# Kernel tuning notes

Hardware: AMD Instinct MI355X
Metric: run time of the kernel (lower is better)

Reference implementation:

```python
import jax, jax.numpy as jnp
import numpy as np

OBS_DIM, ACT_DIM, HID_DIM, FEAT = 256, 32, 1024, 512
T_STEPS, BATCH = 64, 512
LOG2PI = float(np.log(2.0 * np.pi))


def _mlp(h, w0, b0, w1, b1, w2, b2):
    # 2 hidden elu layers + linear head (MLPDecoder mean; fix_std Normal, std=1)
    x = jax.nn.elu(h @ w0.T + b0)
    x = jax.nn.elu(x @ w1.T + b1)
    return x @ w2.T + b2


def _gru(x, h, w_ih, w_hh, b_ih, b_hh):
    # torch.nn.GRUCell semantics
    gi = x @ w_ih.T + b_ih
    gh = h @ w_hh.T + b_hh
    i_r, i_z, i_n = jnp.split(gi, 3, axis=-1)
    h_r, h_z, h_n = jnp.split(gh, 3, axis=-1)
    r = jax.nn.sigmoid(i_r + h_r)
    z = jax.nn.sigmoid(i_z + h_z)
    n = jnp.tanh(i_n + r * h_n)
    return (1.0 - z) * n + z * h


def setup_inputs() -> dict:
    key = jax.random.key(0)
    ks = jax.random.split(key, 20)
    d = {}
    d['obs'] = jax.random.normal(ks[0], (T_STEPS, BATCH, OBS_DIM), jnp.float32)
    d['action'] = jax.random.normal(ks[1], (T_STEPS, BATCH, ACT_DIM), jnp.float32)
    d['reward'] = jax.random.normal(ks[2], (T_STEPS, BATCH, 1), jnp.float32)
    in_dim = OBS_DIM + ACT_DIM
    s = lambda fan_in: 1.0 / np.sqrt(fan_in)
    d['gru_w_ih'] = jax.random.normal(ks[3], (3 * HID_DIM, in_dim), jnp.float32) * s(in_dim)
    d['gru_w_hh'] = jax.random.normal(ks[4], (3 * HID_DIM, HID_DIM), jnp.float32) * s(HID_DIM)
    d['gru_b_ih'] = jnp.zeros((3 * HID_DIM,), jnp.float32)
    d['gru_b_hh'] = jnp.zeros((3 * HID_DIM,), jnp.float32)
    for name, out_dim, base in (('obs', OBS_DIM, 5), ('rew', 1, 11)):
        d[f'{name}_w0'] = jax.random.normal(ks[base], (FEAT, HID_DIM), jnp.float32) * s(HID_DIM)
        d[f'{name}_b0'] = jnp.zeros((FEAT,), jnp.float32)
        d[f'{name}_w1'] = jax.random.normal(ks[base + 1], (FEAT, FEAT), jnp.float32) * s(FEAT)
        d[f'{name}_b1'] = jnp.zeros((FEAT,), jnp.float32)
        d[f'{name}_w2'] = jax.random.normal(ks[base + 2], (out_dim, FEAT), jnp.float32) * s(FEAT)
        d[f'{name}_b2'] = jnp.zeros((out_dim,), jnp.float32)
    return d


def reference(obs, action, reward,
              gru_w_ih, gru_w_hh, gru_b_ih, gru_b_hh,
              obs_w0, obs_b0, obs_w1, obs_b1, obs_w2, obs_b2,
              rew_w0, rew_b0, rew_w1, rew_b1, rew_w2, rew_b2):
    T, B = obs.shape[0], obs.shape[1]

    def normal_logprob_sum(x, mean):
        # Normal(mean, std=1): -0.5*(x-mean)^2 - 0.5*log(2*pi), summed
        return -0.5 * jnp.sum((x - mean) ** 2 + LOG2PI)

    h0 = _gru(jnp.concatenate([obs[0], jnp.zeros_like(action[0])], axis=1),
              jnp.zeros((B, HID_DIM), obs.dtype),
              gru_w_ih, gru_w_hh, gru_b_ih, gru_b_hh)

    def step(h, xs):
        obs_t, act_t, rew_t = xs
        obs_mean = _mlp(h, obs_w0, obs_b0, obs_w1, obs_b1, obs_w2, obs_b2)
        lp_obs = normal_logprob_sum(obs_t, obs_mean)
        rew_mean = _mlp(h, rew_w0, rew_b0, rew_w1, rew_b1, rew_w2, rew_b2)
        lp_rew = normal_logprob_sum(rew_t, rew_mean)
        # feed predicted obs (mode) + ground-truth action back into the GRU
        x = jnp.concatenate([obs_mean, act_t], axis=1)
        h_next = _gru(x, h, gru_w_ih, gru_w_hh, gru_b_ih, gru_b_hh)
        return h_next, (obs_mean, rew_mean, lp_obs, lp_rew)

    _, (pre_obs, pre_reward, lp_obs, lp_rew) = jax.lax.scan(
        step, h0, (obs, action, reward))

    denom = jnp.asarray(T * B, obs.dtype)
    pre_obs_loss = -jnp.sum(lp_obs) / denom
    pre_reward_loss = -jnp.sum(lp_rew) / denom
    loss = pre_obs_loss + pre_reward_loss  # action_mimic=False -> action loss is 0
    return loss, pre_obs, pre_reward
```

## Files before the change

kernel.cpp:

```cpp
#include <hip/hip_runtime.h>
#include <stdint.h>

#define T_STEPS 64
#define BATCH   512
#define OBS_DIM 256
#define ACT_DIM 32
#define HID     1024
#define FEAT    512
#define GDIM    3072
#define KIH     288
#define NBLK    256
#define GMEMB   32
#define LOG2PI  1.8378770664093453f
#define HWREG_XCC_ID 14356

typedef __attribute__((ext_vector_type(8))) short  short8;
typedef __attribute__((ext_vector_type(4))) float  floatx4;
typedef __attribute__((ext_vector_type(4))) unsigned int uintx4;
typedef unsigned long long ull;

__device__ __forceinline__ float bf2f(unsigned int u) {
    return __uint_as_float(u << 16);
}
__device__ __forceinline__ unsigned int f2bf(float f) {
    unsigned int u = __float_as_uint(f);
    return (u + 0x7FFFu + ((u >> 16) & 1u)) >> 16;
}
// ... 60 lines not shown
        int prev = __hip_atomic_fetch_add(cnt, 1, __ATOMIC_RELAXED,
                                          __HIP_MEMORY_SCOPE_AGENT);
        if (prev == members * epoch - 1) {
            __hip_atomic_store(gen, epoch, __ATOMIC_RELAXED,
                               __HIP_MEMORY_SCOPE_AGENT);
        } else {
            while (__hip_atomic_load(gen, __ATOMIC_RELAXED,
                                     __HIP_MEMORY_SCOPE_AGENT) < epoch)
                __builtin_amdgcn_s_sleep(2);
        }
        __builtin_amdgcn_fence(__ATOMIC_ACQUIRE, "workgroup");
    }
    __syncthreads();
}

template<bool COH>
__device__ __forceinline__ void s1_stage(const P& p, unsigned short* lds,
                                         int g, int m,
                                         const unsigned short* hbf_r,
                                         unsigned short* Z1_w,
                                         unsigned short* GHb_w) {
    const int tid = threadIdx.x, lane = tid & 63, wv = tid >> 6;
    const int wr = wv & 1, wc = wv >> 1, fr = lane & 15, fq = lane >> 4;
    const int rowg = g * 64, col0 = m * 128;
    unsigned short* ldsA = lds;
    unsigned short* ldsB = lds + 64 * 136;

    floatx4 acc[2][4];
    floatx4 z4 = {0.f, 0.f, 0.f, 0.f};
#pragma unroll
    for (int mi = 0; mi < 2; ++mi)
#pragma unroll
        for (int n = 0; n < 4; ++n) acc[mi][n] = z4;

    const ull* Aq = (const ull*)(hbf_r + (size_t)rowg * HID);
    const unsigned short* Bg = p.Ws1 + (size_t)col0 * HID;

    ull apf[8];
#pragma unroll
    for (int j = 0; j < 8; ++j) { int f = tid + 256 * j;
        apf[j] = a_ld64<COH>(Aq + (size_t)(f >> 5) * 256 + (f & 31)); }
    uintx4 rb0[4], rb1[4];
#pragma unroll
    for (int i = 0; i < 4; ++i) { int c = tid + 256 * i;
        const unsigned short* bp = Bg + (size_t)(c >> 3) * HID + ((c & 7) << 3);
        rb0[i] = __builtin_nontemporal_load((const uintx4*)bp);
        rb1[i] = __builtin_nontemporal_load((const uintx4*)(bp + 64)); }

#define S1_MFMA(ASUB)                                                          \
    {                                                                          \
        _Pragma("unroll")                                                      \
        for (int ks = 0; ks < 2; ++ks) {                                       \
            short8 af[2], bf8[4];                                              \
            _Pragma("unroll")                                                  \
            for (int mi = 0; mi < 2; ++mi)                                     \
                af[mi] = *(const short8*)(ldsA + (wr * 32 + mi * 16 + fr) * 136 + (ASUB) + ks * 32 + fq * 8); \
            _Pragma("unroll")                                                  \
            for (int n = 0; n < 4; ++n)                                        \
                bf8[n] = *(const short8*)(ldsB + (wc * 64 + n * 16 + fr) * 72 + ks * 32 + fq * 8); \
            _Pragma("unroll")                                                  \
            for (int mi = 0; mi < 2; ++mi)                                     \
                _Pragma("unroll")                                              \
                for (int n = 0; n < 4; ++n)                                    \
                    acc[mi][n] = __builtin_amdgcn_mfma_f32_16x16x32_bf16(      \
                        af[mi], bf8[n], acc[mi][n], 0, 0, 0);                  \
        }                                                                      \
    }

    for (int it2 = 0; it2 < 8; ++it2) {
        bar_fast();
#pragma unroll
        for (int j = 0; j < 8; ++j) { int f = tid + 256 * j;
            *(ull*)(ldsA + (size_t)(f >> 5) * 136 + ((f & 31) << 2)) = apf[j]; }
#pragma unroll
        for (int i = 0; i < 4; ++i) { int c = tid + 256 * i;
            *(uintx4*)(ldsB + (c >> 3) * 72 + ((c & 7) << 3)) = rb0[i]; }
        bar_lds();
        if (it2 < 7) {
            int c2 = it2 + 1;
#pragma unroll
            for (int j = 0; j < 8; ++j) { int f = tid + 256 * j;
                apf[j] = a_ld64<COH>(Aq + (size_t)(f >> 5) * 256 + c2 * 32 + (f & 31)); }
            int k0n = (2 * it2 + 2) * 64;
#pragma unroll
            for (int i = 0; i < 4; ++i) { int c = tid + 256 * i;
                rb0[i] = __builtin_nontemporal_load((const uintx4*)
                    (Bg + (size_t)(c >> 3) * HID + k0n + ((c & 7) << 3))); }
        }
        S1_MFMA(0);
        bar_fast();
#pragma unroll
        for (int i = 0; i < 4; ++i) { int c = tid + 256 * i;
            *(uintx4*)(ldsB + (c >> 3) * 72 + ((c & 7) << 3)) = rb1[i]; }
        bar_lds();
        if (it2 < 7) {
            int k0n = (2 * it2 + 3) * 64;
#pragma unroll
            for (int i = 0; i < 4; ++i) { int c = tid + 256 * i;
                rb1[i] = __builtin_nontemporal_load((const uintx4*)
                    (Bg + (size_t)(c >> 3) * HID + k0n + ((c & 7) << 3))); }
        }
        S1_MFMA(64);
    }
#undef S1_MFMA

    const bool isZ1 = (col0 < 1024);
#pragma unroll
    for (int mi = 0; mi < 2; ++mi)
#pragma unroll
        for (int n = 0; n < 4; ++n)
#pragma unroll
            for (int j = 0; j < 4; ++j) {
                int row = rowg + wr * 32 + mi * 16 + fq * 4 + j;
                int col = col0 + wc * 64 + n * 16 + fr;
                float v = acc[mi][n][j] + p.bias_s1[col];
                unsigned int ow = f2bf(isZ1 ? elu1(v) : v);
                unsigned int pr = __shfl_xor(ow, 1, 64);
                if (!(fr & 1)) {
                    unsigned int pk = ow | (pr << 16);
                    if (isZ1)
                        a_st<COH>((unsigned int*)(Z1_w + row * HID + col), pk);
                    else
                        a_st<COH>((unsigned int*)GHb_w + (size_t)row * 1536 + ((col - 1024) >> 1), pk);
                }
            }
}

template<bool COH>
__device__ __forceinline__ void s2_stage(const P& p, unsigned short* lds,
                                         int g, int m,
                                         const unsigned short* Z1_r,
                                         unsigned short* Z2_w) {
    const int tid = threadIdx.x, lane = tid & 63, wv = tid >> 6;
    const int wr = wv & 1, wc = wv >> 1, fr = lane & 15, fq = lane >> 4;
    const int rowg = g * 64;
    const int z = m >> 4, col0 = (m & 15) * 32;
    unsigned short* ldsA = lds;
    unsigned short* ldsB = lds + 64 * 136;

    floatx4 acc[2];
    floatx4 z4 = {0.f, 0.f, 0.f, 0.f};
    acc[0] = z4; acc[1] = z4;

    const ull* Aq = (const ull*)(Z1_r + (size_t)rowg * HID + z * FEAT);
    const unsigned short* Bg = (z ? p.W1r : p.W1o) + (size_t)col0 * FEAT;
    const float* bias = z ? p.b1r : p.b1o;

    ull apf[8];
#pragma unroll
    for (int j = 0; j < 8; ++j) { int f = tid + 256 * j;
        apf[j] = a_ld64<COH>(Aq + (size_t)(f >> 5) * 256 + (f & 31)); }
    const unsigned short* bp0 = Bg + (size_t)(tid >> 3) * FEAT + ((tid & 7) << 3);
    uintx4 rb0 = *(const uintx4*)(bp0);
    uintx4 rb1 = *(const uintx4*)(bp0 + 64);

#define S2_MFMA(ASUB)                                                          \
    {                                                                          \
        _Pragma("unroll")                                                      \
        for (int ks = 0; ks < 2; ++ks) {                                       \
            short8 bf8 = *(const short8*)(ldsB + (wc * 16 + fr) * 72 + ks * 32 + fq * 8); \
            _Pragma("unroll")                                                  \
            for (int mi = 0; mi < 2; ++mi) {                                   \
                short8 af = *(const short8*)(ldsA + (wr * 32 + mi * 16 + fr) * 136 + (ASUB) + ks * 32 + fq * 8); \
                acc[mi] = __builtin_amdgcn_mfma_f32_16x16x32_bf16(af, bf8, acc[mi], 0, 0, 0); \
            }                                                                  \
        }                                                                      \
    }

    for (int it2 = 0; it2 < 4; ++it2) {
        bar_fast();
#pragma unroll
        for (int j = 0; j < 8; ++j) { int f = tid + 256 * j;
            *(ull*)(ldsA + (size_t)(f >> 5) * 136 + ((f & 31) << 2)) = apf[j]; }
        *(uintx4*)(ldsB + (tid >> 3) * 72 + ((tid & 7) << 3)) = rb0;
        bar_lds();
        if (it2 < 3) {
            int c2 = it2 + 1;
#pragma unroll
            for (int j = 0; j < 8; ++j) { int f = tid + 256 * j;
                apf[j] = a_ld64<COH>(Aq + (size_t)(f >> 5) * 256 + c2 * 32 + (f & 31)); }
            rb0 = *(const uintx4*)(bp0 + (2 * it2 + 2) * 64);
        }
        S2_MFMA(0);
        bar_fast();
        *(uintx4*)(ldsB + (tid >> 3) * 72 + ((tid & 7) << 3)) = rb1;
        bar_lds();
        if (it2 < 3) rb1 = *(const uintx4*)(bp0 + (2 * it2 + 3) * 64);
        S2_MFMA(64);
    }
#undef S2_MFMA

#pragma unroll
    for (int mi = 0; mi < 2; ++mi)
#pragma unroll
        for (int j = 0; j < 4; ++j) {
            int row = rowg + wr * 32 + mi * 16 + fq * 4 + j;
            int col = col0 + wc * 16 + fr;
            float v = acc[mi][j] + bias[col];
            unsigned int ow = f2bf(elu1(v));
            unsigned int pr = __shfl_xor(ow, 1, 64);
            if (!(fr & 1))
                a_st<COH>((unsigned int*)(Z2_w + row * HID + z * FEAT + col), ow | (pr << 16));
        }
}

template<bool COH>
__device__ __forceinline__ void s3_stage(const P& p, unsigned short* lds,
                                         int g, int m, int t,
                                         const unsigned short* Z2_r,
                                         unsigned short* Xbuf_w) {
    const int tid = threadIdx.x, lane = tid & 63, wv = tid >> 6;
    const int wr = wv & 1, wc = wv >> 1, fr = lane & 15, fq = lane >> 4;
    const int rowg = g * 64;

    if (m < 8) {
        const int col0 = m * 32;
        unsigned short* ldsA = lds;
        unsigned short* ldsB = lds + 64 * 136;
        floatx4 acc[2];
        floatx4 z4 = {0.f, 0.f, 0.f, 0.f};
        acc[0] = z4; acc[1] = z4;

        const ull* Aq = (const ull*)(Z2_r + (size_t)rowg * HID);
        const unsigned short* Bg = p.W2o + (size_t)col0 * FEAT;

        ull apf[8];
#pragma unroll
        for (int j = 0; j < 8; ++j) { int f = tid + 256 * j;
            apf[j] = a_ld64<COH>(Aq + (size_t)(f >> 5) * 256 + (f & 31)); }
        const unsigned short* bp0 = Bg + (size_t)(tid >> 3) * FEAT + ((tid & 7) << 3);
        uintx4 rb0 = *(const uintx4*)(bp0);
        uintx4 rb1 = *(const uintx4*)(bp0 + 64);

#define S3_MFMA(ASUB)                                                          \
        {                                                                      \
            _Pragma("unroll")                                                  \
            for (int ks = 0; ks < 2; ++ks) {                                   \
                short8 bf8 = *(const short8*)(ldsB + (wc * 16 + fr) * 72 + ks * 32 + fq * 8); \
                _Pragma("unroll")                                              \
                for (int mi = 0; mi < 2; ++mi) {                               \
                    short8 af = *(const short8*)(ldsA + (wr * 32 + mi * 16 + fr) * 136 + (ASUB) + ks * 32 + fq * 8); \
                    acc[mi] = __builtin_amdgcn_mfma_f32_16x16x32_bf16(af, bf8, acc[mi], 0, 0, 0); \
                }                                                              \
            }                                                                  \
        }

        for (int it2 = 0; it2 < 4; ++it2) {
            bar_fast();
#pragma unroll
            for (int j = 0; j < 8; ++j) { int f = tid + 256 * j;
                *(ull*)(ldsA + (size_t)(f >> 5) * 136 + ((f & 31) << 2)) = apf[j]; }
            *(uintx4*)(ldsB + (tid >> 3) * 72 + ((tid & 7) << 3)) = rb0;
            bar_lds();
            if (it2 < 3) {
                int c2 = it2 + 1;
#pragma unroll
                for (int j = 0; j < 8; ++j) { int f = tid + 256 * j;
                    apf[j] = a_ld64<COH>(Aq + (size_t)(f >> 5) * 256 + c2 * 32 + (f & 31)); }
                rb0 = *(const uintx4*)(bp0 + (2 * it2 + 2) * 64);
            }
            S3_MFMA(0);
            bar_fast();
            *(uintx4*)(ldsB + (tid >> 3) * 72 + ((tid & 7) << 3)) = rb1;
            bar_lds();
            if (it2 < 3) rb1 = *(const uintx4*)(bp0 + (2 * it2 + 3) * 64);
            S3_MFMA(64);
        }
#undef S3_MFMA

        const int col = col0 + wc * 16 + fr;
        const float b2oc = p.b2o[col];
        float lsum = 0.f;
#pragma unroll
        for (int mi = 0; mi < 2; ++mi)
#pragma unroll
            for (int j = 0; j < 4; ++j) {
                int row = rowg + wr * 32 + mi * 16 + fq * 4 + j;
                float mval = acc[mi][j] + b2oc;
                size_t oidx = (size_t)t * BATCH * OBS_DIM + (size_t)row * OBS_DIM + col;
                __builtin_nontemporal_store(mval, p.out + 1 + oidx);
                unsigned int ow = f2bf(mval);
                unsigned int pr = __shfl_xor(ow, 1, 64);
                if (!(fr & 1))
                    a_st<COH>((unsigned int*)(Xbuf_w + row * KIH + col), ow | (pr << 16));
                float d = __builtin_nontemporal_load(p.obs + oidx) - mval;
                lsum += d * d;
            }
#pragma unroll
        for (int off = 32; off > 0; off >>= 1) lsum += __shfl_down(lsum, off, 64);
        if (lane == 0) atomicAdd(p.accum + 0, lsum);
    } else if (m == 8) {
        for (int e = tid; e < 64 * 16; e += 256) {
            int row = rowg + (e >> 4), cp = (e & 15) * 2;
            const float* ap = p.action + ((size_t)t * BATCH + row) * ACT_DIM + cp;
            unsigned int lo = f2bf(__builtin_nontemporal_load(ap));
            unsigned int hi = f2bf(__builtin_nontemporal_load(ap + 1));
            a_st<COH>((unsigned int*)(Xbuf_w + row * KIH + OBS_DIM + cp), lo | (hi << 16));
        }
    } else if (m >= 16) {
        const int row = rowg + (m - 16) * 4 + wv;
        const ull* zq = (const ull*)(Z2_r + (size_t)row * HID + FEAT) + lane * 2;
        ull z0 = a_ld64<COH>(zq);
        ull z1 = a_ld64<COH>(zq + 1);
        short8 w8 = *(const short8*)(p.w2r + lane * 8);
        float s = 0.f;
#pragma unroll
        for (int k = 0; k < 4; ++k) {
            unsigned int u = (unsigned int)(z0 >> (16 * k)) & 0xFFFFu;
            s += bf2f(u) * bf2f((unsigned int)(unsigned short)w8[k]);
        }
#pragma unroll
        for (int k = 0; k < 4; ++k) {
            unsigned int u = (unsigned int)(z1 >> (16 * k)) & 0xFFFFu;
            s += bf2f(u) * bf2f((unsigned int)(unsigned short)w8[4 + k]);
// ... 6 lines not shown
                mm, p.out + 1 + (size_t)T_STEPS * BATCH * OBS_DIM + (size_t)t * BATCH + row);
            float d = __builtin_nontemporal_load(p.reward + (size_t)t * BATCH + row) - mm;
            atomicAdd(p.accum + 1, d * d);
        }
    }
}

template<bool COH>
__device__ __forceinline__ void s4_stage(const P& p, unsigned short* lds,
                                         int g, int m, int use_gh,
                                         const unsigned short* Xbuf_r,
                                         const unsigned short* GHb_r,
                                         const float* h_r,
                                         float* h_w, unsigned short* hbf_w) {
    const int tid = threadIdx.x, lane = tid & 63, wv = tid >> 6;
    const int wr = wv & 1, wc = wv >> 1, fr = lane & 15, fq = lane >> 4;
    const int rowg = g * 64;
    const int col0 = m * 32;
    unsigned short* ldsA = lds;
    unsigned short* ldsB = lds + 64 * 104;

    floatx4 acc[3][2];
    floatx4 z4 = {0.f, 0.f, 0.f, 0.f};
#pragma unroll
    for (int g3 = 0; g3 < 3; ++g3) { acc[g3][0] = z4; acc[g3][1] = z4; }

    const ull* Xq = (const ull*)(Xbuf_r + (size_t)rowg * KIH);
    ull apf[6];
#pragma unroll
    for (int j = 0; j < 6; ++j) { int f = tid + 256 * j;
        apf[j] = a_ld64<COH>(Xq + (size_t)(f / 24) * 72 + (f % 24)); }

    uintx4 wpfA[5], wpfB[5];
#pragma unroll
    for (int j = 0; j < 5; ++j) { int f = tid + 256 * j;
        if (f < 1152) { int r = f / 12, ko = (f - r * 12) * 8;
            const unsigned short* wp =
                p.Wih + (size_t)((r >> 5) * HID + col0 + (r & 31)) * KIH + ko;
            wpfA[j] = __builtin_nontemporal_load((const uintx4*)wp);
            wpfB[j] = __builtin_nontemporal_load((const uintx4*)(wp + 96)); } }

#pragma unroll
    for (int c = 0; c < 3; ++c) {
        bar_fast();
#pragma unroll
        for (int j = 0; j < 6; ++j) { int f = tid + 256 * j;
            *(ull*)(ldsA + (size_t)(f / 24) * 104 + ((f % 24) << 2)) = apf[j]; }
#pragma unroll
        for (int j = 0; j < 5; ++j) { int f = tid + 256 * j;
            if (f < 1152) { int r = f / 12, ko = (f - r * 12) * 8;
                *(uintx4*)(ldsB + r * 104 + ko) = (c & 1) ? wpfB[j] : wpfA[j]; } }
        bar_lds();
        if (c < 2) {
#pragma unroll
            for (int j = 0; j < 6; ++j) { int f = tid + 256 * j;
                apf[j] = a_ld64<COH>(Xq + (size_t)(f / 24) * 72 + (c + 1) * 24 + (f % 24)); }
        }
        if (c == 0) {
#pragma unroll
            for (int j = 0; j < 5; ++j) { int f = tid + 256 * j;
                if (f < 1152) { int r = f / 12, ko = (f - r * 12) * 8;
                    wpfA[j] = __builtin_nontemporal_load((const uintx4*)
                        (p.Wih + (size_t)((r >> 5) * HID + col0 + (r & 31)) * KIH + 192 + ko)); } }
        }
#pragma unroll
        for (int ks = 0; ks < 3; ++ks) {
            short8 af[2];
#pragma unroll
            for (int mi = 0; mi < 2; ++mi)
                af[mi] = *(const short8*)(ldsA + (wr * 32 + mi * 16 + fr) * 104 + ks * 32 + fq * 8);
#pragma unroll
            for (int g3 = 0; g3 < 3; ++g3) {
                short8 bf8 = *(const short8*)(ldsB + (g3 * 32 + wc * 16 + fr) * 104 + ks * 32 + fq * 8);
#pragma unroll
                for (int mi = 0; mi < 2; ++mi)
                    acc[g3][mi] = __builtin_amdgcn_mfma_f32_16x16x32_bf16(
                        af[mi], bf8, acc[g3][mi], 0, 0, 0);
            }
        }
    }

    const int col = col0 + wc * 16 + fr;
    const float bir = p.b_ih[col];
    const float biz = p.b_ih[HID + col];
    const float bin = p.b_ih[2 * HID + col];
    float hrv[2][4], hzv[2][4], hnv[2][4], hpv[2][4];
    if (use_gh) {
        const unsigned int* GW = (const unsigned int*)GHb_r;
        const int cw = col >> 1, hi = col & 1;
#pragma unroll
        for (int mi = 0; mi < 2; ++mi)
#pragma unroll
            for (int j = 0; j < 4; ++j) {
                int row = rowg + wr * 32 + mi * 16 + fq * 4 + j;
                unsigned int ur = a_ld<COH>(GW + (size_t)row * 1536 + cw);
                unsigned int uz = a_ld<COH>(GW + (size_t)row * 1536 + 512 + cw);
                unsigned int un = a_ld<COH>(GW + (size_t)row * 1536 + 1024 + cw);
                hrv[mi][j] = bf2f(hi ? (ur >> 16) : (ur & 0xFFFFu));
                hzv[mi][j] = bf2f(hi ? (uz >> 16) : (uz & 0xFFFFu));
                hnv[mi][j] = bf2f(hi ? (un >> 16) : (un & 0xFFFFu));
                hpv[mi][j] = __uint_as_float(a_ld<COH>((const unsigned int*)(h_r + (size_t)row * HID + col)));
            }
    } else {
        float br = p.b_hh[col], bz = p.b_hh[HID + col], bn = p.b_hh[2 * HID + col];
#pragma unroll
        for (int mi = 0; mi < 2; ++mi)
#pragma unroll
            for (int j = 0; j < 4; ++j) {
                hrv[mi][j] = br; hzv[mi][j] = bz; hnv[mi][j] = bn; hpv[mi][j] = 0.f;
            }
    }
#pragma unroll
    for (int mi = 0; mi < 2; ++mi)
#pragma unroll
        for (int j = 0; j < 4; ++j) {
            int row = rowg + wr * 32 + mi * 16 + fq * 4 + j;
            float r  = sigm(acc[0][mi][j] + bir + hrv[mi][j]);
            float z  = sigm(acc[1][mi][j] + biz + hzv[mi][j]);
            float nn = tanhf(acc[2][mi][j] + bin + r * hnv[mi][j]);
            float hv = (1.f - z) * nn + z * hpv[mi][j];
            a_st<COH>((unsigned int*)(h_w + (size_t)row * HID + col), __float_as_uint(hv));
            unsigned int ow = f2bf(hv);
            unsigned int pr = __shfl_xor(ow, 1, 64);
            if (!(fr & 1))
                a_st<COH>((unsigned int*)(hbf_w + row * HID + col), ow | (pr << 16));
        }
}

template<bool COH>
__device__ void rollout(const P& p, unsigned short* lds, int g, int m) {
    int* gcnt = p.bar + g * 128;
    int* ggen = p.bar + g * 128 + 64;
    int epoch = 0;

    s4_stage<COH>(p, lds, g, m, 0, p.Xbuf[1], p.GHb[0], p.h[0], p.h[0], p.hbf[0]);
    gbar(gcnt, ggen, epoch, GMEMB);

    for (int t = 0; t < T_STEPS; ++t) {
        const int pr = t & 1, nx = (t + 1) & 1;
        s1_stage<COH>(p, lds, g, m, p.hbf[pr], p.Z1[pr], p.GHb[pr]);
        gbar(gcnt, ggen, epoch, GMEMB);
        s2_stage<COH>(p, lds, g, m, p.Z1[pr], p.Z2[pr]);
        gbar(gcnt, ggen, epoch, GMEMB);
        s3_stage<COH>(p, lds, g, m, t, p.Z2[pr], p.Xbuf[pr]);
        gbar(gcnt, ggen, epoch, GMEMB);
        if (t < T_STEPS - 1) {
            s4_stage<COH>(p, lds, g, m, 1, p.Xbuf[pr], p.GHb[pr], p.h[pr],
                          p.h[nx], p.hbf[nx]);
            gbar(gcnt, ggen, epoch, GMEMB);
        }
    }
}

__global__ __launch_bounds__(256, 1) void k_persist(P p) {
    __shared__ unsigned short lds[17920];
    __shared__ int sh[3];

    const int bid = blockIdx.x;
    if (threadIdx.x == 0) {
        unsigned int xcd = __builtin_amdgcn_s_getreg(HWREG_XCC_ID) & 7u;
        int r = __hip_atomic_fetch_add(p.bar + 1024 + xcd, 1,
                                       __ATOMIC_RELAXED, __HIP_MEMORY_SCOPE_AGENT);
        sh[0] = (int)xcd; sh[1] = r;
    }
    int repoch = 0;
    gbar(p.bar + 1200, p.bar + 1264, repoch, NBLK);
    if (threadIdx.x == 0) {
        int ok = (sh[1] < 32);
        for (int i = 0; i < 8; ++i)
            ok &= (dev_ld((const unsigned int*)(p.bar + 1024 + i)) == 32u);
        sh[2] = ok;
    }
    __syncthreads();

    if (sh[2]) rollout<false>(p, lds, sh[0], sh[1]);
    else       rollout<true >(p, lds, bid & 7, bid >> 3);

    gbar(p.bar + 1200, p.bar + 1264, repoch, NBLK);
    if (bid == 0 && threadIdx.x == 0) {
        const float inv = 1.f / (float)(T_STEPS * BATCH);
        float a0 = dev_ldf(p.accum + 0);
        float a1 = dev_ldf(p.accum + 1);
        p.out[0] = 0.5f * a0 * inv + 128.f * LOG2PI
                 + 0.5f * a1 * inv + 0.5f * LOG2PI;
    }
}

__global__ void k_convert(
    const float* __restrict__ ow0, const float* __restrict__ rw0,
    const float* __restrict__ whh, const float* __restrict__ wih,
    const float* __restrict__ ow1, const float* __restrict__ rw1,
    const float* __restrict__ ow2, const float* __restrict__ rw2,
    const float* __restrict__ ob0, const float* __restrict__ rb0,
    const float* __restrict__ bhh,
// ... 21 lines not shown
    for (int i = i0; i < 4096; i += stride)
        bias_s1[i] = (i < 512) ? ob0[i] : (i < 1024) ? rb0[i - 512] : bhh[i - 1024];
}

__global__ void k_init(const float* __restrict__ obs,
                       unsigned short* __restrict__ Xbuf1,
                       float* __restrict__ accum,
                       int* __restrict__ bar)
{
    int i = blockIdx.x * 256 + threadIdx.x;
    if (i < BATCH * KIH) {
        int row = i / KIH, col = i - row * KIH;
        Xbuf1[i] = (col < OBS_DIM) ? (unsigned short)f2bf(obs[row * OBS_DIM + col])
                                   : (unsigned short)0;
    }
    if (i < 2)    accum[i] = 0.f;
    if (i < 1536) bar[i] = 0;
}

extern "C" void kernel_launch(void* const* d_in, const int* in_sizes, int n_in,
                              void* d_out, int out_size, void* d_ws, size_t ws_size,
                              hipStream_t stream)
{
    const float* obs      = (const float*)d_in[0];
    const float* action   = (const float*)d_in[1];
    const float* reward   = (const float*)d_in[2];
    const float* gru_w_ih = (const float*)d_in[3];
    const float* gru_w_hh = (const float*)d_in[4];
    const float* gru_b_ih = (const float*)d_in[5];
    const float* gru_b_hh = (const float*)d_in[6];
    const float* obs_w0   = (const float*)d_in[7];
    const float* obs_b0   = (const float*)d_in[8];
// ... 22 lines not shown
    unsigned short* w2r  = (unsigned short*)alloc((size_t)FEAT * 2);
    float* bias_s1       = (float*)alloc((size_t)4096 * 4);
    unsigned short* Z1a  = (unsigned short*)alloc((size_t)BATCH * HID * 2);
    unsigned short* Z1b  = (unsigned short*)alloc((size_t)BATCH * HID * 2);
    unsigned short* Z2a  = (unsigned short*)alloc((size_t)BATCH * HID * 2);
    unsigned short* Z2b  = (unsigned short*)alloc((size_t)BATCH * HID * 2);
    unsigned short* GHa  = (unsigned short*)alloc((size_t)BATCH * GDIM * 2);
    unsigned short* GHbB = (unsigned short*)alloc((size_t)BATCH * GDIM * 2);
    unsigned short* Xba  = (unsigned short*)alloc((size_t)BATCH * KIH * 2);
    unsigned short* Xbb  = (unsigned short*)alloc((size_t)BATCH * KIH * 2);
    float* ha            = (float*)alloc((size_t)BATCH * HID * 4);
    float* hb            = (float*)alloc((size_t)BATCH * HID * 4);
    unsigned short* hfa  = (unsigned short*)alloc((size_t)BATCH * HID * 2);
    unsigned short* hfb  = (unsigned short*)alloc((size_t)BATCH * HID * 2);
    float* accum         = (float*)alloc(256);
    int*   bar           = (int*)alloc(8192);

    dim3 blk(256);

    k_convert<<<dim3(1024), blk, 0, stream>>>(
        obs_w0, rew_w0, gru_w_hh, gru_w_ih, obs_w1, rew_w1, obs_w2, rew_w2,
        obs_b0, rew_b0, gru_b_hh, Ws1, Wih, W1o, W1r, W2o, w2r, bias_s1);

    k_init<<<dim3((BATCH * KIH + 255) / 256), blk, 0, stream>>>(obs, Xbb, accum, bar);

    P hp;
    hp.obs = obs; hp.action = action; hp.reward = reward;
    hp.b_ih = gru_b_ih; hp.b_hh = gru_b_hh;
    hp.b1o = obs_b1; hp.b1r = rew_b1; hp.b2o = obs_b2; hp.b2r = rew_b2;
    hp.Ws1 = Ws1; hp.Wih = Wih; hp.W1o = W1o; hp.W1r = W1r;
    hp.W2o = W2o; hp.w2r = w2r; hp.bias_s1 = bias_s1;
    hp.Z1[0] = Z1a; hp.Z1[1] = Z1b;
    hp.Z2[0] = Z2a; hp.Z2[1] = Z2b;
    hp.Xbuf[0] = Xba; hp.Xbuf[1] = Xbb;
    hp.hbf[0] = hfa; hp.hbf[1] = hfb;
    hp.GHb[0] = GHa; hp.GHb[1] = GHbB;
    hp.h[0] = ha; hp.h[1] = hb;
    hp.accum = accum; hp.out = (float*)d_out;
    hp.bar = bar;

    k_persist<<<dim3(NBLK), blk, 0, stream>>>(hp);
}
```

Measured before the change: 2.542 ms.

## Double persistent blocks to 512 with 32-row tiles and flag-based group barriers

Measured after the change: 3.772 ms. +48.4%, slower.

```diff
diff --git a/kernel.cpp b/kernel.cpp
--- a/kernel.cpp
+++ b/kernel.cpp
@@ -9,8 +9,7 @@
 #define FEAT    512
 #define GDIM    3072
 #define KIH     288
-#define NBLK    256
-#define GMEMB   32
+#define NBLK    512
 #define LOG2PI  1.8378770664093453f
 #define HWREG_XCC_ID 14356
 
@@ -101,31 +100,60 @@
     __syncthreads();
 }
 
+__device__ __forceinline__ void gbar_flags(int* fbase, int m, int& epoch) {
+    __syncthreads();
+    epoch++;
+    if (threadIdx.x == 0) {
+        __builtin_amdgcn_fence(__ATOMIC_RELEASE, "workgroup");
+        dev_st((unsigned int*)(fbase + m * 16), (unsigned int)epoch);
+    }
+    if (threadIdx.x < 64) {
+        const unsigned int* fp =
+            (const unsigned int*)(fbase + (threadIdx.x & 31) * 16);
+        while ((int)dev_ld(fp) < epoch) __builtin_amdgcn_s_sleep(4);
+        __builtin_amdgcn_fence(__ATOMIC_ACQUIRE, "workgroup");
+    }
+    __syncthreads();
+}
+
+__device__ __forceinline__ void gbar_all(int* fbase, int a, int& epoch) {
+    __syncthreads();
+    epoch++;
+    if (threadIdx.x == 0) {
+        __builtin_amdgcn_fence(__ATOMIC_RELEASE, "workgroup");
+        dev_st((unsigned int*)(fbase + a * 16), (unsigned int)epoch);
+    }
+    {
+        const unsigned int* fp =
+            (const unsigned int*)(fbase + threadIdx.x * 16);
+        while ((int)dev_ld(fp) < epoch) __builtin_amdgcn_s_sleep(4);
+    }
+    __builtin_amdgcn_fence(__ATOMIC_ACQUIRE, "workgroup");
+    __syncthreads();
+}
+
 template<bool COH>
 __device__ __forceinline__ void s1_stage(const P& p, unsigned short* lds,
                                          int g, int m,
                                          const unsigned short* hbf_r,
                                          unsigned short* Z1_w,
                                          unsigned short* GHb_w) {
-    const int tid = threadIdx.x, lane = tid & 63, wv = tid >> 6;
-    const int wr = wv & 1, wc = wv >> 1, fr = lane & 15, fq = lane >> 4;
-    const int rowg = g * 64, col0 = m * 128;
+    const int tid = threadIdx.x, lane = tid & 63, wc = tid >> 6;
+    const int fr = lane & 15, fq = lane >> 4;
+    const int rowg = g * 32, col0 = m * 128;
     unsigned short* ldsA = lds;
-    unsigned short* ldsB = lds + 64 * 136;
-
-    floatx4 acc[2][4];
+    unsigned short* ldsB = lds + 32 * 136;
+
+    floatx4 acc[2][2];
     floatx4 z4 = {0.f, 0.f, 0.f, 0.f};
-#pragma unroll
-    for (int mi = 0; mi < 2; ++mi)
-#pragma unroll
-        for (int n = 0; n < 4; ++n) acc[mi][n] = z4;
+    acc[0][0] = z4; acc[0][1] = z4; acc[1][0] = z4; acc[1][1] = z4;
 
     const ull* Aq = (const ull*)(hbf_r + (size_t)rowg * HID);
     const unsigned short* Bg = p.Ws1 + (size_t)col0 * HID;
 
-    ull apf[8];
-#pragma unroll
-    for (int j = 0; j < 8; ++j) { int f = tid + 256 * j;
+    ull apf[4];
+#pragma unroll
+    for (int j = 0; j < 4; ++j) { int f = tid + 256 * j;
         apf[j] = a_ld64<COH>(Aq + (size_t)(f >> 5) * 256 + (f & 31)); }
     uintx4 rb0[4], rb1[4];
 #pragma unroll
@@ -136,28 +164,30 @@
 
 #define S1_MFMA(ASUB)                                                          \
     {                                                                          \
+        __builtin_amdgcn_s_setprio(1);                                         \
         _Pragma("unroll")                                                      \
         for (int ks = 0; ks < 2; ++ks) {                                       \
-            short8 af[2], bf8[4];                                              \
+            short8 af[2], bf8[2];                                              \
             _Pragma("unroll")                                                  \
             for (int mi = 0; mi < 2; ++mi)                                     \
-                af[mi] = *(const short8*)(ldsA + (wr * 32 + mi * 16 + fr) * 136 + (ASUB) + ks * 32 + fq * 8); \
+                af[mi] = *(const short8*)(ldsA + (mi * 16 + fr) * 136 + (ASUB) + ks * 32 + fq * 8); \
             _Pragma("unroll")                                                  \
-            for (int n = 0; n < 4; ++n)                                        \
-                bf8[n] = *(const short8*)(ldsB + (wc * 64 + n * 16 + fr) * 72 + ks * 32 + fq * 8); \
+            for (int n = 0; n < 2; ++n)                                        \
+                bf8[n] = *(const short8*)(ldsB + (wc * 32 + n * 16 + fr) * 72 + ks * 32 + fq * 8); \
             _Pragma("unroll")                                                  \
             for (int mi = 0; mi < 2; ++mi)                                     \
                 _Pragma("unroll")                                              \
-                for (int n = 0; n < 4; ++n)                                    \
+                for (int n = 0; n < 2; ++n)                                    \
                     acc[mi][n] = __builtin_amdgcn_mfma_f32_16x16x32_bf16(      \
                         af[mi], bf8[n], acc[mi][n], 0, 0, 0);                  \
         }                                                                      \
+        __builtin_amdgcn_s_setprio(0);                                         \
     }
 
     for (int it2 = 0; it2 < 8; ++it2) {
         bar_fast();
 #pragma unroll
-        for (int j = 0; j < 8; ++j) { int f = tid + 256 * j;
+        for (int j = 0; j < 4; ++j) { int f = tid + 256 * j;
             *(ull*)(ldsA + (size_t)(f >> 5) * 136 + ((f & 31) << 2)) = apf[j]; }
 #pragma unroll
         for (int i = 0; i < 4; ++i) { int c = tid + 256 * i;
@@ -166,7 +196,7 @@
         if (it2 < 7) {
             int c2 = it2 + 1;
 #pragma unroll
-            for (int j = 0; j < 8; ++j) { int f = tid + 256 * j;
+            for (int j = 0; j < 4; ++j) { int f = tid + 256 * j;
                 apf[j] = a_ld64<COH>(Aq + (size_t)(f >> 5) * 256 + c2 * 32 + (f & 31)); }
             int k0n = (2 * it2 + 2) * 64;
 #pragma unroll
@@ -195,11 +225,11 @@
 #pragma unroll
     for (int mi = 0; mi < 2; ++mi)
 #pragma unroll
-        for (int n = 0; n < 4; ++n)
+        for (int n = 0; n < 2; ++n)
 #pragma unroll
             for (int j = 0; j < 4; ++j) {
-                int row = rowg + wr * 32 + mi * 16 + fq * 4 + j;
-                int col = col0 + wc * 64 + n * 16 + fr;
+                int row = rowg + mi * 16 + fq * 4 + j;
+                int col = col0 + wc * 32 + n * 16 + fr;
                 float v = acc[mi][n][j] + p.bias_s1[col];
                 unsigned int ow = f2bf(isZ1 ? elu1(v) : v);
                 unsigned int pr = __shfl_xor(ow, 1, 64);
@@ -219,76 +249,67 @@
                                          const unsigned short* Z1_r,
                                          unsigned short* Z2_w) {
     const int tid = threadIdx.x, lane = tid & 63, wv = tid >> 6;
-    const int wr = wv & 1, wc = wv >> 1, fr = lane & 15, fq = lane >> 4;
-    const int rowg = g * 64;
+    const int wr = wv & 1, wc = wv >> 1;
+    const int fr = lane & 15, fq = lane >> 4;
+    const int rowg = g * 32;
     const int z = m >> 4, col0 = (m & 15) * 32;
     unsigned short* ldsA = lds;
-    unsigned short* ldsB = lds + 64 * 136;
-
-    floatx4 acc[2];
-    floatx4 z4 = {0.f, 0.f, 0.f, 0.f};
-    acc[0] = z4; acc[1] = z4;
+    unsigned short* ldsB = lds + 32 * 136;
+
+    floatx4 acc = {0.f, 0.f, 0.f, 0.f};
 
     const ull* Aq = (const ull*)(Z1_r + (size_t)rowg * HID + z * FEAT);
     const unsigned short* Bg = (z ? p.W1r : p.W1o) + (size_t)col0 * FEAT;
     const float* bias = z ? p.b1r : p.b1o;
 
-    ull apf[8];
-#pragma unroll
-    for (int j = 0; j < 8; ++j) { int f = tid + 256 * j;
+    ull apf[4];
+#pragma unroll
+    for (int j = 0; j < 4; ++j) { int f = tid + 256 * j;
         apf[j] = a_ld64<COH>(Aq + (size_t)(f >> 5) * 256 + (f & 31)); }
     const unsigned short* bp0 = Bg + (size_t)(tid >> 3) * FEAT + ((tid & 7) << 3);
     uintx4 rb0 = *(const uintx4*)(bp0);
     uintx4 rb1 = *(const uintx4*)(bp0 + 64);
 
-#define S2_MFMA(ASUB)                                                          \
-    {                                                                          \
-        _Pragma("unroll")                                                      \
-        for (int ks = 0; ks < 2; ++ks) {                                       \
-            short8 bf8 = *(const short8*)(ldsB + (wc * 16 + fr) * 72 + ks * 32 + fq * 8); \
-            _Pragma("unroll")                                                  \
-            for (int mi = 0; mi < 2; ++mi) {                                   \
-                short8 af = *(const short8*)(ldsA + (wr * 32 + mi * 16 + fr) * 136 + (ASUB) + ks * 32 + fq * 8); \
-                acc[mi] = __builtin_amdgcn_mfma_f32_16x16x32_bf16(af, bf8, acc[mi], 0, 0, 0); \
-            }                                                                  \
-        }                                                                      \
-    }
+#define S23_MFMA(ASUB)                                                         \
+    { _Pragma("unroll")                                                        \
+      for (int ks = 0; ks < 2; ++ks) {                                         \
+        short8 bf8 = *(const short8*)(ldsB + (wc * 16 + fr) * 72 + ks * 32 + fq * 8); \
+        short8 af = *(const short8*)(ldsA + (wr * 16 + fr) * 136 + (ASUB) + ks * 32 + fq * 8); \
+        acc = __builtin_amdgcn_mfma_f32_16x16x32_bf16(af, bf8, acc, 0, 0, 0);  \
+      } }
 
     for (int it2 = 0; it2 < 4; ++it2) {
         bar_fast();
 #pragma unroll
-        for (int j = 0; j < 8; ++j) { int f = tid + 256 * j;
+        for (int j = 0; j < 4; ++j) { int f = tid + 256 * j;
             *(ull*)(ldsA + (size_t)(f >> 5) * 136 + ((f & 31) << 2)) = apf[j]; }
         *(uintx4*)(ldsB + (tid >> 3) * 72 + ((tid & 7) << 3)) = rb0;
         bar_lds();
         if (it2 < 3) {
             int c2 = it2 + 1;
 #pragma unroll
-            for (int j = 0; j < 8; ++j) { int f = tid + 256 * j;
+            for (int j = 0; j < 4; ++j) { int f = tid + 256 * j;
                 apf[j] = a_ld64<COH>(Aq + (size_t)(f >> 5) * 256 + c2 * 32 + (f & 31)); }
             rb0 = *(const uintx4*)(bp0 + (2 * it2 + 2) * 64);
         }
-        S2_MFMA(0);
+        S23_MFMA(0);
         bar_fast();
         *(uintx4*)(ldsB + (tid >> 3) * 72 + ((tid & 7) << 3)) = rb1;
         bar_lds();
         if (it2 < 3) rb1 = *(const uintx4*)(bp0 + (2 * it2 + 3) * 64);
-        S2_MFMA(64);
-    }
-#undef S2_MFMA
-
-#pragma unroll
-    for (int mi = 0; mi < 2; ++mi)
-#pragma unroll
-        for (int j = 0; j < 4; ++j) {
-            int row = rowg + wr * 32 + mi * 16 + fq * 4 + j;
-            int col = col0 + wc * 16 + fr;
-            float v = acc[mi][j] + bias[col];
-            unsigned int ow = f2bf(elu1(v));
-            unsigned int pr = __shfl_xor(ow, 1, 64);
-            if (!(fr & 1))
-                a_st<COH>((unsigned int*)(Z2_w + row * HID + z * FEAT + col), ow | (pr << 16));
-        }
+        S23_MFMA(64);
+    }
+
+#pragma unroll
+    for (int j = 0; j < 4; ++j) {
+        int row = rowg + wr * 16 + fq * 4 + j;
+        int col = col0 + wc * 16 + fr;
+        float v = acc[j] + bias[col];
+        unsigned int ow = f2bf(elu1(v));
+        unsigned int pr = __shfl_xor(ow, 1, 64);
+        if (!(fr & 1))
+            a_st<COH>((unsigned int*)(Z2_w + row * HID + z * FEAT + col), ow | (pr << 16));
+    }
 }
 
 template<bool COH>
@@ -297,94 +318,77 @@
                                          const unsigned short* Z2_r,
                                          unsigned short* Xbuf_w) {
     const int tid = threadIdx.x, lane = tid & 63, wv = tid >> 6;
-    const int wr = wv & 1, wc = wv >> 1, fr = lane & 15, fq = lane >> 4;
-    const int rowg = g * 64;
+    const int wr = wv & 1, wc = wv >> 1;
+    const int fr = lane & 15, fq = lane >> 4;
+    const int rowg = g * 32;
 
     if (m < 8) {
         const int col0 = m * 32;
         unsigned short* ldsA = lds;
-        unsigned short* ldsB = lds + 64 * 136;
-        floatx4 acc[2];
-        floatx4 z4 = {0.f, 0.f, 0.f, 0.f};
-        acc[0] = z4; acc[1] = z4;
+        unsigned short* ldsB = lds + 32 * 136;
+        floatx4 acc = {0.f, 0.f, 0.f, 0.f};
 
         const ull* Aq = (const ull*)(Z2_r + (size_t)rowg * HID);
         const unsigned short* Bg = p.W2o + (size_t)col0 * FEAT;
 
-        ull apf[8];
-#pragma unroll
-        for (int j = 0; j < 8; ++j) { int f = tid + 256 * j;
+        ull apf[4];
+#pragma unroll
+        for (int j = 0; j < 4; ++j) { int f = tid + 256 * j;
             apf[j] = a_ld64<COH>(Aq + (size_t)(f >> 5) * 256 + (f & 31)); }
         const unsigned short* bp0 = Bg + (size_t)(tid >> 3) * FEAT + ((tid & 7) << 3);
         uintx4 rb0 = *(const uintx4*)(bp0);
         uintx4 rb1 = *(const uintx4*)(bp0 + 64);
 
-#define S3_MFMA(ASUB)                                                          \
-        {                                                                      \
-            _Pragma("unroll")                                                  \
-            for (int ks = 0; ks < 2; ++ks) {                                   \
-                short8 bf8 = *(const short8*)(ldsB + (wc * 16 + fr) * 72 + ks * 32 + fq * 8); \
-                _Pragma("unroll")                                              \
-                for (int mi = 0; mi < 2; ++mi) {                               \
-                    short8 af = *(const short8*)(ldsA + (wr * 32 + mi * 16 + fr) * 136 + (ASUB) + ks * 32 + fq * 8); \
-                    acc[mi] = __builtin_amdgcn_mfma_f32_16x16x32_bf16(af, bf8, acc[mi], 0, 0, 0); \
-                }                                                              \
-            }                                                                  \
-        }
-
         for (int it2 = 0; it2 < 4; ++it2) {
             bar_fast();
 #pragma unroll
-            for (int j = 0; j < 8; ++j) { int f = tid + 256 * j;
+            for (int j = 0; j < 4; ++j) { int f = tid + 256 * j;
                 *(ull*)(ldsA + (size_t)(f >> 5) * 136 + ((f & 31) << 2)) = apf[j]; }
             *(uintx4*)(ldsB + (tid >> 3) * 72 + ((tid & 7) << 3)) = rb0;
             bar_lds();
             if (it2 < 3) {
                 int c2 = it2 + 1;
 #pragma unroll
-                for (int j = 0; j < 8; ++j) { int f = tid + 256 * j;
+                for (int j = 0; j < 4; ++j) { int f = tid + 256 * j;
                     apf[j] = a_ld64<COH>(Aq + (size_t)(f >> 5) * 256 + c2 * 32 + (f & 31)); }
                 rb0 = *(const uintx4*)(bp0 + (2 * it2 + 2) * 64);
             }
-            S3_MFMA(0);
+            S23_MFMA(0);
             bar_fast();
             *(uintx4*)(ldsB + (tid >> 3) * 72 + ((tid & 7) << 3)) = rb1;
             bar_lds();
             if (it2 < 3) rb1 = *(const uintx4*)(bp0 + (2 * it2 + 3) * 64);
-            S3_MFMA(64);
-        }
-#undef S3_MFMA
+            S23_MFMA(64);
+        }
 
         const int col = col0 + wc * 16 + fr;
         const float b2oc = p.b2o[col];
         float lsum = 0.f;
 #pragma unroll
-        for (int mi = 0; mi < 2; ++mi)
-#pragma unroll
-            for (int j = 0; j < 4; ++j) {
-                int row = rowg + wr * 32 + mi * 16 + fq * 4 + j;
-                float mval = acc[mi][j] + b2oc;
-                size_t oidx = (size_t)t * BATCH * OBS_DIM + (size_t)row * OBS_DIM + col;
-                __builtin_nontemporal_store(mval, p.out + 1 + oidx);
-                unsigned int ow = f2bf(mval);
-                unsigned int pr = __shfl_xor(ow, 1, 64);
-                if (!(fr & 1))
-                    a_st<COH>((unsigned int*)(Xbuf_w + row * KIH + col), ow | (pr << 16));
-                float d = __builtin_nontemporal_load(p.obs + oidx) - mval;
-                lsum += d * d;
-            }
+        for (int j = 0; j < 4; ++j) {
+            int row = rowg + wr * 16 + fq * 4 + j;
+            float mval = acc[j] + b2oc;
+            size_t oidx = (size_t)t * BATCH * OBS_DIM + (size_t)row * OBS_DIM + col;
+            __builtin_nontemporal_store(mval, p.out + 1 + oidx);
+            unsigned int ow = f2bf(mval);
+            unsigned int pr = __shfl_xor(ow, 1, 64);
+            if (!(fr & 1))
+                a_st<COH>((unsigned int*)(Xbuf_w + row * KIH + col), ow | (pr << 16));
+            float d = __builtin_nontemporal_load(p.obs + oidx) - mval;
+            lsum += d * d;
+        }
 #pragma unroll
         for (int off = 32; off > 0; off >>= 1) lsum += __shfl_down(lsum, off, 64);
         if (lane == 0) atomicAdd(p.accum + 0, lsum);
     } else if (m == 8) {
-        for (int e = tid; e < 64 * 16; e += 256) {
+        for (int e = tid; e < 32 * 16; e += 256) {
             int row = rowg + (e >> 4), cp = (e & 15) * 2;
             const float* ap = p.action + ((size_t)t * BATCH + row) * ACT_DIM + cp;
             unsigned int lo = f2bf(__builtin_nontemporal_load(ap));
             unsigned int hi = f2bf(__builtin_nontemporal_load(ap + 1));
             a_st<COH>((unsigned int*)(Xbuf_w + row * KIH + OBS_DIM + cp), lo | (hi << 16));
         }
-    } else if (m >= 16) {
+    } else if (m >= 16 && m < 24) {
         const int row = rowg + (m - 16) * 4 + wv;
         const ull* zq = (const ull*)(Z2_r + (size_t)row * HID + FEAT) + lane * 2;
         ull z0 = a_ld64<COH>(zq);
@@ -421,22 +425,22 @@
                                          const float* h_r,
                                          float* h_w, unsigned short* hbf_w) {
     const int tid = threadIdx.x, lane = tid & 63, wv = tid >> 6;
-    const int wr = wv & 1, wc = wv >> 1, fr = lane & 15, fq = lane >> 4;
-    const int rowg = g * 64;
+    const int wr = wv & 1, wc = wv >> 1;
+    const int fr = lane & 15, fq = lane >> 4;
+    const int rowg = g * 32;
     const int col0 = m * 32;
     unsigned short* ldsA = lds;
-    unsigned short* ldsB = lds + 64 * 104;
-
-    floatx4 acc[3][2];
+    unsigned short* ldsB = lds + 32 * 104;
+
+    floatx4 acc[3];
     floatx4 z4 = {0.f, 0.f, 0.f, 0.f};
-#pragma unroll
-    for (int g3 = 0; g3 < 3; ++g3) { acc[g3][0] = z4; acc[g3][1] = z4; }
+    acc[0] = z4; acc[1] = z4; acc[2] = z4;
 
     const ull* Xq = (const ull*)(Xbuf_r + (size_t)rowg * KIH);
-    ull apf[6];
-#pragma unroll
-    for (int j = 0; j < 6; ++j) { int f = tid + 256 * j;
-        apf[j] = a_ld64<COH>(Xq + (size_t)(f / 24) * 72 + (f % 24)); }
+    ull apf[3];
+#pragma unroll
+    for (int j = 0; j < 3; ++j) { int f = tid + 256 * j;
+        if (f < 768) apf[j] = a_ld64<COH>(Xq + (size_t)(f / 24) * 72 + (f % 24)); }
 
     uintx4 wpfA[5], wpfB[5];
 #pragma unroll
@@ -451,8 +455,8 @@
     for (int c = 0; c < 3; ++c) {
         bar_fast();
 #pragma unroll
-        for (int j = 0; j < 6; ++j) { int f = tid + 256 * j;
-            *(ull*)(ldsA + (size_t)(f / 24) * 104 + ((f % 24) << 2)) = apf[j]; }
+        for (int j = 0; j < 3; ++j) { int f = tid + 256 * j;
+            if (f < 768) *(ull*)(ldsA + (size_t)(f / 24) * 104 + ((f % 24) << 2)) = apf[j]; }
 #pragma unroll
         for (int j = 0; j < 5; ++j) { int f = tid + 256 * j;
             if (f < 1152) { int r = f / 12, ko = (f - r * 12) * 8;
@@ -460,8 +464,8 @@
         bar_lds();
         if (c < 2) {
 #pragma unroll
-            for (int j = 0; j < 6; ++j) { int f = tid + 256 * j;
-                apf[j] = a_ld64<COH>(Xq + (size_t)(f / 24) * 72 + (c + 1) * 24 + (f % 24)); }
+            for (int j = 0; j < 3; ++j) { int f = tid + 256 * j;
+                if (f < 768) apf[j] = a_ld64<COH>(Xq + (size_t)(f / 24) * 72 + (c + 1) * 24 + (f % 24)); }
         }
         if (c == 0) {
 #pragma unroll
@@ -472,17 +476,11 @@
         }
 #pragma unroll
         for (int ks = 0; ks < 3; ++ks) {
-            short8 af[2];
-#pragma unroll
-            for (int mi = 0; mi < 2; ++mi)
-                af[mi] = *(const short8*)(ldsA + (wr * 32 + mi * 16 + fr) * 104 + ks * 32 + fq * 8);
+            short8 af = *(const short8*)(ldsA + (wr * 16 + fr) * 104 + ks * 32 + fq * 8);
 #pragma unroll
             for (int g3 = 0; g3 < 3; ++g3) {
                 short8 bf8 = *(const short8*)(ldsB + (g3 * 32 + wc * 16 + fr) * 104 + ks * 32 + fq * 8);
-#pragma unroll
-                for (int mi = 0; mi < 2; ++mi)
-                    acc[g3][mi] = __builtin_amdgcn_mfma_f32_16x16x32_bf16(
-                        af[mi], bf8, acc[g3][mi], 0, 0, 0);
+                acc[g3] = __builtin_amdgcn_mfma_f32_16x16x32_bf16(af, bf8, acc[g3], 0, 0, 0);
             }
         }
     }
@@ -491,100 +489,145 @@
     const float bir = p.b_ih[col];
     const float biz = p.b_ih[HID + col];
     const float bin = p.b_ih[2 * HID + col];
-    float hrv[2][4], hzv[2][4], hnv[2][4], hpv[2][4];
+    float hrv[4], hzv[4], hnv[4], hpv[4];
     if (use_gh) {
         const unsigned int* GW = (const unsigned int*)GHb_r;
         const int cw = col >> 1, hi = col & 1;
 #pragma unroll
-        for (int mi = 0; mi < 2; ++mi)
-#pragma unroll
-            for (int j = 0; j < 4; ++j) {
-                int row = rowg + wr * 32 + mi * 16 + fq * 4 + j;
-                unsigned int ur = a_ld<COH>(GW + (size_t)row * 1536 + cw);
-                unsigned int uz = a_ld<COH>(GW + (size_t)row * 1536 + 512 + cw);
-                unsigned int un = a_ld<COH>(GW + (size_t)row * 1536 + 1024 + cw);
-                hrv[mi][j] = bf2f(hi ? (ur >> 16) : (ur & 0xFFFFu));
-                hzv[mi][j] = bf2f(hi ? (uz >> 16) : (uz & 0xFFFFu));
-                hnv[mi][j] = bf2f(hi ? (un >> 16) : (un & 0xFFFFu));
-                hpv[mi][j] = __uint_as_float(a_ld<COH>((const unsigned int*)(h_r + (size_t)row * HID + col)));
-            }
+        for (int j = 0; j < 4; ++j) {
+            int row = rowg + wr * 16 + fq * 4 + j;
+            unsigned int ur = a_ld<COH>(GW + (size_t)row * 1536 + cw);
+            unsigned int uz = a_ld<COH>(GW + (size_t)row * 1536 + 512 + cw);
+            unsigned int un = a_ld<COH>(GW + (size_t)row * 1536 + 1024 + cw);
+            hrv[j] = bf2f(hi ? (ur >> 16) : (ur & 0xFFFFu));
+            hzv[j] = bf2f(hi ? (uz >> 16) : (uz & 0xFFFFu));
+            hnv[j] = bf2f(hi ? (un >> 16) : (un & 0xFFFFu));
+            hpv[j] = __uint_as_float(a_ld<COH>((const unsigned int*)(h_r + (size_t)row * HID + col)));
+        }
     } else {
         float br = p.b_hh[col], bz = p.b_hh[HID + col], bn = p.b_hh[2 * HID + col];
 #pragma unroll
-        for (int mi = 0; mi < 2; ++mi)
-#pragma unroll
-            for (int j = 0; j < 4; ++j) {
-                hrv[mi][j] = br; hzv[mi][j] = bz; hnv[mi][j] = bn; hpv[mi][j] = 0.f;
-            }
-    }
-#pragma unroll
-    for (int mi = 0; mi < 2; ++mi)
-#pragma unroll
         for (int j = 0; j < 4; ++j) {
-            int row = rowg + wr * 32 + mi * 16 + fq * 4 + j;
-            float r  = sigm(acc[0][mi][j] + bir + hrv[mi][j]);
-            float z  = sigm(acc[1][mi][j] + biz + hzv[mi][j]);
-            float nn = tanhf(acc[2][mi][j] + bin + r * hnv[mi][j]);
-            float hv = (1.f - z) * nn + z * hpv[mi][j];
-            a_st<COH>((unsigned int*)(h_w + (size_t)row * HID + col), __float_as_uint(hv));
-            unsigned int ow = f2bf(hv);
-            unsigned int pr = __shfl_xor(ow, 1, 64);
-            if (!(fr & 1))
-                a_st<COH>((unsigned int*)(hbf_w + row * HID + col), ow | (pr << 16));
-        }
+            hrv[j] = br; hzv[j] = bz; hnv[j] = bn; hpv[j] = 0.f;
+        }
+    }
+#pragma unroll
+    for (int j = 0; j < 4; ++j) {
+        int row = rowg + wr * 16 + fq * 4 + j;
+        float r  = sigm(acc[0][j] + bir + hrv[j]);
+        float z  = sigm(acc[1][j] + biz + hzv[j]);
+        float nn = tanhf(acc[2][j] + bin + r * hnv[j]);
+        float hv = (1.f - z) * nn + z * hpv[j];
+        a_st<COH>((unsigned int*)(h_w + (size_t)row * HID + col), __float_as_uint(hv));
+        unsigned int ow = f2bf(hv);
+        unsigned int pr = __shfl_xor(ow, 1, 64);
+        if (!(fr & 1))
+            a_st<COH>((unsigned int*)(hbf_w + row * HID + col), ow | (pr << 16));
+    }
 }
 
 template<bool COH>
 __device__ void rollout(const P& p, unsigned short* lds, int g, int m) {
-    int* gcnt = p.bar + g * 128;
-    int* ggen = p.bar + g * 128 + 64;
-    int epoch = 0;
+    int* fbase = p.bar + 2048 + g * 512;
+    int fep = 0;
 
     s4_stage<COH>(p, lds, g, m, 0, p.Xbuf[1], p.GHb[0], p.h[0], p.h[0], p.hbf[0]);
-    gbar(gcnt, ggen, epoch, GMEMB);
+    gbar_flags(fbase, m, fep);
 
     for (int t = 0; t < T_STEPS; ++t) {
         const int pr = t & 1, nx = (t + 1) & 1;
         s1_stage<COH>(p, lds, g, m, p.hbf[pr], p.Z1[pr], p.GHb[pr]);
-        gbar(gcnt, ggen, epoch, GMEMB);
+        gbar_flags(fbase, m, fep);
         s2_stage<COH>(p, lds, g, m, p.Z1[pr], p.Z2[pr]);
-        gbar(gcnt, ggen, epoch, GMEMB);
+        gbar_flags(fbase, m, fep);
         s3_stage<COH>(p, lds, g, m, t, p.Z2[pr], p.Xbuf[pr]);
-        gbar(gcnt, ggen, epoch, GMEMB);
+        gbar_flags(fbase, m, fep);
         if (t < T_STEPS - 1) {
             s4_stage<COH>(p, lds, g, m, 1, p.Xbuf[pr], p.GHb[pr], p.h[pr],
                           p.h[nx], p.hbf[nx]);
-            gbar(gcnt, ggen, epoch, GMEMB);
-        }
-    }
-}
-
-__global__ __launch_bounds__(256, 1) void k_persist(P p) {
-    __shared__ unsigned short lds[17920];
-    __shared__ int sh[3];
-
-    const int bid = blockIdx.x;
+            gbar_flags(fbase, m, fep);
+        }
+    }
+}
+
+__device__ void rollout_dual(const P& p, unsigned short* lds,
+                             int g0, int g1, int m, int a) {
+    int* fb = p.bar + 10240;
+    int fep = 0;
+
+    s4_stage<true>(p, lds, g0, m, 0, p.Xbuf[1], p.GHb[0], p.h[0], p.h[0], p.hbf[0]);
+    s4_stage<true>(p, lds, g1, m, 0, p.Xbuf[1], p.GHb[0], p.h[0], p.h[0], p.hbf[0]);
+    gbar_all(fb, a, fep);
+
+    for (int t = 0; t < T_STEPS; ++t) {
+        const int pr = t & 1, nx = (t + 1) & 1;
+        s1_stage<true>(p, lds, g0, m, p.hbf[pr], p.Z1[pr], p.GHb[pr]);
+        s1_stage<true>(p, lds, g1, m, p.hbf[pr], p.Z1[pr], p.GHb[pr]);
+        gbar_all(fb, a, fep);
+        s2_stage<true>(p, lds, g0, m, p.Z1[pr], p.Z2[pr]);
+        s2_stage<true>(p, lds, g1, m, p.Z1[pr], p.Z2[pr]);
+        gbar_all(fb, a, fep);
+        s3_stage<true>(p, lds, g0, m, t, p.Z2[pr], p.Xbuf[pr]);
+        s3_stage<true>(p, lds, g1, m, t, p.Z2[pr], p.Xbuf[pr]);
+        gbar_all(fb, a, fep);
+        if (t < T_STEPS - 1) {
+            s4_stage<true>(p, lds, g0, m, 1, p.Xbuf[pr], p.GHb[pr], p.h[pr],
+                           p.h[nx], p.hbf[nx]);
+            s4_stage<true>(p, lds, g1, m, 1, p.Xbuf[pr], p.GHb[pr], p.h[pr],
+                           p.h[nx], p.hbf[nx]);
+            gbar_all(fb, a, fep);
+        }
+    }
+}
+
+__global__ __launch_bounds__(256, 2) void k_persist(P p) {
+    __shared__ unsigned short lds[27648];
+    __shared__ int sh[4];
+
     if (threadIdx.x == 0) {
         unsigned int xcd = __builtin_amdgcn_s_getreg(HWREG_XCC_ID) & 7u;
-        int r = __hip_atomic_fetch_add(p.bar + 1024 + xcd, 1,
-                                       __ATOMIC_RELAXED, __HIP_MEMORY_SCOPE_AGENT);
-        sh[0] = (int)xcd; sh[1] = r;
-    }
-    int repoch = 0;
-    gbar(p.bar + 1200, p.bar + 1264, repoch, NBLK);
-    if (threadIdx.x == 0) {
-        int ok = (sh[1] < 32);
-        for (int i = 0; i < 8; ++i)
-            ok &= (dev_ld((const unsigned int*)(p.bar + 1024 + i)) == 32u);
-        sh[2] = ok;
+        int rx = __hip_atomic_fetch_add(p.bar + 1024 + xcd, 1,
+                                        __ATOMIC_RELAXED, __HIP_MEMORY_SCOPE_AGENT);
+        int a  = __hip_atomic_fetch_add(p.bar + 1088, 1,
+                                        __ATOMIC_RELAXED, __HIP_MEMORY_SCOPE_AGENT);
+        if (a == 0) {
+            ull t0 = (ull)__builtin_amdgcn_s_memrealtime();
+            int c;
+            for (;;) {
+                c = (int)dev_ld((const unsigned int*)(p.bar + 1088));
+                if (c >= NBLK) break;
+                if ((ull)__builtin_amdgcn_s_memrealtime() - t0 > 400000ull) break;
+                __builtin_amdgcn_s_sleep(16);
+            }
+            dev_st((unsigned int*)(p.bar + 1092), (c >= NBLK) ? 1u : 2u);
+        }
+        unsigned int mode;
+        while ((mode = dev_ld((const unsigned int*)(p.bar + 1092))) == 0u)
+            __builtin_amdgcn_s_sleep(16);
+        int ok = 0;
+        if (mode == 1u) {
+            ok = (rx < 64);
+            for (int i = 0; i < 8; ++i)
+                ok &= (dev_ld((const unsigned int*)(p.bar + 1024 + i)) == 64u);
+        }
+        sh[0] = (int)xcd; sh[1] = rx; sh[2] = (int)mode | (ok << 8); sh[3] = a;
     }
     __syncthreads();
-
-    if (sh[2]) rollout<false>(p, lds, sh[0], sh[1]);
-    else       rollout<true >(p, lds, bid & 7, bid >> 3);
-
-    gbar(p.bar + 1200, p.bar + 1264, repoch, NBLK);
-    if (bid == 0 && threadIdx.x == 0) {
+    const int xcd = sh[0], rx = sh[1], a = sh[3];
+    const int mode = sh[2] & 0xFF, ok = sh[2] >> 8;
+
+    int eep = 0;
+    if (mode == 1) {
+        if (ok) rollout<false>(p, lds, xcd * 2 + (rx >> 5), rx & 31);
+        else    rollout<true >(p, lds, a >> 5, a & 31);
+        gbar(p.bar + 1104, p.bar + 1168, eep, NBLK);
+    } else {
+        if (a >= 256) return;
+        rollout_dual(p, lds, a >> 5, 8 + (a >> 5), a & 31, a);
+        gbar(p.bar + 1104, p.bar + 1168, eep, 256);
+    }
+
+    if (a == 0 && threadIdx.x == 0) {
         const float inv = 1.f / (float)(T_STEPS * BATCH);
         float a0 = dev_ldf(p.accum + 0);
         float a1 = dev_ldf(p.accum + 1);
@@ -636,8 +679,8 @@
         Xbuf1[i] = (col < OBS_DIM) ? (unsigned short)f2bf(obs[row * OBS_DIM + col])
                                    : (unsigned short)0;
     }
-    if (i < 2)    accum[i] = 0.f;
-    if (i < 1536) bar[i] = 0;
+    if (i < 2)     accum[i] = 0.f;
+    if (i < 16384) bar[i] = 0;
 }
 
 extern "C" void kernel_launch(void* const* d_in, const int* in_sizes, int n_in,
@@ -690,15 +733,13 @@
     unsigned short* hfa  = (unsigned short*)alloc((size_t)BATCH * HID * 2);
     unsigned short* hfb  = (unsigned short*)alloc((size_t)BATCH * HID * 2);
     float* accum         = (float*)alloc(256);
-    int*   bar           = (int*)alloc(8192);
-
-    dim3 blk(256);
-
-    k_convert<<<dim3(1024), blk, 0, stream>>>(
+    int*   bar           = (int*)alloc(65536);
+
+    k_convert<<<dim3(1024), dim3(256), 0, stream>>>(
         obs_w0, rew_w0, gru_w_hh, gru_w_ih, obs_w1, rew_w1, obs_w2, rew_w2,
         obs_b0, rew_b0, gru_b_hh, Ws1, Wih, W1o, W1r, W2o, w2r, bias_s1);
 
-    k_init<<<dim3((BATCH * KIH + 255) / 256), blk, 0, stream>>>(obs, Xbb, accum, bar);
+    k_init<<<dim3((BATCH * KIH + 255) / 256), dim3(256), 0, stream>>>(obs, Xbb, accum, bar);
 
     P hp;
     hp.obs = obs; hp.action = action; hp.reward = reward;
@@ -715,5 +756,5 @@
     hp.accum = accum; hp.out = (float*)d_out;
     hp.bar = bar;
 
-    k_persist<<<dim3(NBLK), blk, 0, stream>>>(hp);
-}
+    k_persist<<<dim3(NBLK), dim3(256), 0, stream>>>(hp);
+}
```
